# Performance work log

Hardware: AMD Instinct MI355X
Metric: run time of the kernel (lower is better)

Reference implementation:

```python
import jax, jax.numpy as jnp
import numpy as np

N = 2048

def setup_inputs() -> dict:
    key = jax.random.key(0)
    ks = jax.random.split(key, 7)
    x = jax.random.uniform(ks[0], (N,), dtype=jnp.float32) * 100.0  # time vector
    W1 = jax.random.normal(ks[1], (128, 2), dtype=jnp.float32) * 0.5
    b1 = jax.random.normal(ks[2], (128,), dtype=jnp.float32) * 0.1
    W2 = jax.random.normal(ks[3], (32, 128), dtype=jnp.float32) * 0.1
    b2 = jax.random.normal(ks[4], (32,), dtype=jnp.float32) * 0.1
    W3 = jax.random.normal(ks[5], (1, 32), dtype=jnp.float32) * 0.1
    b3 = jax.random.normal(ks[6], (1,), dtype=jnp.float32) * 0.1
    return {"x": x, "W1": W1, "b1": b1, "W2": W2, "b2": b2, "W3": W3, "b3": b3}

def reference(x, W1, b1, W2, b2, W3, b3):
    # Vectorized equivalent of the nested-loop pair build:
    # pairs (x[i], x[j]) for all j >= i (upper triangle incl. diagonal).
    n = x.shape[0]
    iu_r, iu_c = np.triu_indices(n)  # static index arrays, P = n(n+1)/2
    pairs = jnp.stack([x[iu_r], x[iu_c]], axis=-1)  # [P, 2]
    h = jax.nn.sigmoid(pairs @ W1.T + b1)           # [P, 128]
    h = jax.nn.relu(h @ W2.T + b2)                  # [P, 32]
    v = (h @ W3.T + b3)[:, 0]                       # [P]
    # K starts as eye; the loops overwrite the full upper triangle (incl. diag),
    # leaving the strictly-lower triangle at 0.
    K = jnp.zeros((n, n), dtype=x.dtype).at[iu_r, iu_c].set(v)
    return K.T @ K  # torch casts to double; kept float32 (jax x64 disabled)
```

## Files before the change

kernel.cpp:

```cpp
#include <hip/hip_runtime.h>
#include <hip/hip_bf16.h>

#define N 2048

using f32x4  = __attribute__((ext_vector_type(4))) float;
using short8 = __attribute__((ext_vector_type(8))) short;

#define GLOAD_LDS16(dst, src)                                                        \
  __builtin_amdgcn_global_load_lds((const __attribute__((address_space(1))) void*)(src), \
                                   (__attribute__((address_space(3))) void*)(dst), 16, 0, 0)

__device__ __forceinline__ short f2bf(float f) {
  unsigned u = __builtin_bit_cast(unsigned, f);
  u += 0x7fffu + ((u >> 16) & 1u);
  return (short)(u >> 16);
}

__global__ void w2_to_bf16(const float* __restrict__ W2, __hip_bfloat16* __restrict__ W2b) {
  int t = blockIdx.x * 256 + threadIdx.x;
  W2b[t] = __float2bfloat16(W2[t]);
}

__global__ __launch_bounds__(256) void build_A_mfma(
    const float* __restrict__ x,
    const float* __restrict__ W1,
    const float* __restrict__ b1,
    const __hip_bfloat16* __restrict__ W2b,
    const float* __restrict__ b2,
    const float* __restrict__ W3,
    const float* __restrict__ b3,
    __hip_bfloat16* __restrict__ A)
{
  const int bi = blockIdx.x, bj = blockIdx.y;
  const int i0 = bi * 16, j0 = bj * 16;
  const int tid = threadIdx.x;

  if (bi > bj) {
    A[(size_t)(j0 + (tid >> 4)) * N + i0 + (tid & 15)] = __float2bfloat16(0.0f);
    return;
  }

  __shared__ float w1s[256];
  __shared__ float b1s[128];
  w1s[tid] = W1[tid];
  if (tid < 128) b1s[tid] = b1[tid];
  __syncthreads();

  const int w  = tid >> 6;
  const int l  = tid & 63;
  const int lm = l & 15;
  const int lk = l >> 4;

  const float xi = x[i0 + lm];
  float xj[4];
#pragma unroll
  for (int m = 0; m < 4; ++m) xj[m] = x[j0 + w * 4 + m];

  short8 wf[2][4];
#pragma unroll
  for (int g = 0; g < 2; ++g)
#pragma unroll
    for (int kb = 0; kb < 4; ++kb)
      wf[g][kb] = *(const short8*)(W2b + (g * 16 + lm) * 128 + kb * 32 + lk * 8);

  float b2v[2] = {b2[lm], b2[16 + lm]};
  f32x4 acc[4][2];
#pragma unroll
  for (int m = 0; m < 4; ++m)
#pragma unroll
    for (int g = 0; g < 2; ++g)
      acc[m][g] = (f32x4){b2v[g], b2v[g], b2v[g], b2v[g]};

  for (int kb = 0; kb < 4; ++kb) {
    float w1a[8], w1b[8], bb[8];
#pragma unroll
    for (int e = 0; e < 8; ++e) {
      const int k = kb * 32 + lk * 8 + e;
      w1a[e] = w1s[2 * k];
      w1b[e] = w1s[2 * k + 1];
      bb[e]  = b1s[k];
    }
#pragma unroll
    for (int m = 0; m < 4; ++m) {
      short8 af;
#pragma unroll
      for (int e = 0; e < 8; ++e) {
        const float t  = fmaf(w1a[e], xi, fmaf(w1b[e], xj[m], bb[e]));
        const float ex = __expf(-t);
        const float h  = __builtin_amdgcn_rcpf(1.0f + ex);
        af[e] = f2bf(h);
      }
      acc[m][0] = __builtin_amdgcn_mfma_f32_16x16x32_bf16(af, wf[0][kb], acc[m][0], 0, 0, 0);
      acc[m][1] = __builtin_amdgcn_mfma_f32_16x16x32_bf16(af, wf[1][kb], acc[m][1], 0, 0, 0);
    }
  }

  const float w3a = W3[lm], w3b = W3[16 + lm];
  const float b3v = b3[0];
  const int   rsel = l & 3;

#pragma unroll
  for (int m = 0; m < 4; ++m) {
    const int j = j0 + w * 4 + m;
    float v[4];
#pragma unroll
    for (int r = 0; r < 4; ++r) {
      float s = fmaf(fmaxf(acc[m][0][r], 0.0f), w3a,
                     fmaxf(acc[m][1][r], 0.0f) * w3b);
      s += __shfl_xor(s, 1);
      s += __shfl_xor(s, 2);
      s += __shfl_xor(s, 4);
      s += __shfl_xor(s, 8);
      v[r] = s + b3v;
    }
    const float sv = rsel == 0 ? v[0] : rsel == 1 ? v[1] : rsel == 2 ? v[2] : v[3];
    if (lm < 4) {
      const int i = i0 + lk * 4 + rsel;
      A[(size_t)j * N + i] = (i <= j) ? __float2bfloat16(sv) : __float2bfloat16(0.0f);
    }
  }
}

__global__ __launch_bounds__(256) void gemm_ata(
    const __hip_bfloat16* __restrict__ A, float* __restrict__ C)
{
  __shared__ __align__(16) __hip_bfloat16 As[128 * 32];
  __shared__ __align__(16) __hip_bfloat16 Bs[128 * 32];

  const int m0 = blockIdx.y * 128;
  const int n0 = blockIdx.x * 128;
  const int tid = threadIdx.x;
  const int w  = tid >> 6;
  const int l  = tid & 63;
  const int wr = (w >> 1) * 64;
  const int wc = (w & 1) * 64;
  const int lm = l & 15;
  const int lk = l >> 4;

  f32x4 acc[4][4];
#pragma unroll
  for (int m = 0; m < 4; ++m)
#pragma unroll
    for (int n = 0; n < 4; ++n)
      acc[m][n] = (f32x4){0.f, 0.f, 0.f, 0.f};

  const int mn = m0 < n0 ? m0 : n0;
  const int ktiles = (mn + 128) >> 5;

  const int srow = l >> 2;
  const int scol = (l & 3) * 8;

  for (int kt = 0; kt < ktiles; ++kt) {
    const int k0 = kt * 32;
    __syncthreads();
#pragma unroll
    for (int c = 0; c < 2; ++c) {
      const int r0 = (w * 2 + c) * 16;
      const __hip_bfloat16* ga = A + (size_t)(m0 + r0 + srow) * N + k0 + scol;
      const __hip_bfloat16* gb = A + (size_t)(n0 + r0 + srow) * N + k0 + scol;
      GLOAD_LDS16(As + r0 * 32, ga);
      GLOAD_LDS16(Bs + r0 * 32, gb);
    }
    __syncthreads();

    short8 af[4], bfr[4];
#pragma unroll
    for (int m = 0; m < 4; ++m)
      af[m] = *(const short8*)(As + (wr + m * 16 + lm) * 32 + lk * 8);
#pragma unroll
    for (int n = 0; n < 4; ++n)
      bfr[n] = *(const short8*)(Bs + (wc + n * 16 + lm) * 32 + lk * 8);

#pragma unroll
    for (int m = 0; m < 4; ++m)
#pragma unroll
      for (int n = 0; n < 4; ++n)
        acc[m][n] = __builtin_amdgcn_mfma_f32_16x16x32_bf16(af[m], bfr[n], acc[m][n], 0, 0, 0);
  }

#pragma unroll
  for (int m = 0; m < 4; ++m) {
    const int row = m0 + wr + m * 16 + lk * 4;
#pragma unroll
    for (int n = 0; n < 4; ++n) {
      const int col = n0 + wc + n * 16 + lm;
#pragma unroll
      for (int r = 0; r < 4; ++r)
        C[(size_t)(row + r) * N + col] = acc[m][n][r];
    }
  }
}

extern "C" void kernel_launch(void* const* d_in, const int* in_sizes, int n_in,
                              void* d_out, int out_size, void* d_ws, size_t ws_size,
                              hipStream_t stream) {
  const float* x  = (const float*)d_in[0];
  const float* W1 = (const float*)d_in[1];
  const float* b1 = (const float*)d_in[2];
  const float* W2 = (const float*)d_in[3];
  const float* b2 = (const float*)d_in[4];
  const float* W3 = (const float*)d_in[5];
  const float* b3 = (const float*)d_in[6];
  float* C = (float*)d_out;

  __hip_bfloat16* W2b = (__hip_bfloat16*)d_ws;
  __hip_bfloat16* A   = (__hip_bfloat16*)((char*)d_ws + 16384);

  w2_to_bf16<<<dim3(16), dim3(256), 0, stream>>>(W2, W2b);
  build_A_mfma<<<dim3(N / 16, N / 16), dim3(256), 0, stream>>>(x, W1, b1, W2b, b2, W3, b3, A);
  gemm_ata<<<dim3(N / 128, N / 128), dim3(256), 0, stream>>>(A, C);
}
```

Baseline: 219.4 us.

## Triangular grid for A build, prescaled sigmoid, separate zero pass, smaller GEMM tiles

```diff
diff --git a/kernel.cpp b/kernel.cpp
--- a/kernel.cpp
+++ b/kernel.cpp
@@ -5,45 +5,50 @@
 
 using f32x4  = __attribute__((ext_vector_type(4))) float;
 using short8 = __attribute__((ext_vector_type(8))) short;
+using uint4v = __attribute__((ext_vector_type(4))) unsigned int;
 
 #define GLOAD_LDS16(dst, src)                                                        \
   __builtin_amdgcn_global_load_lds((const __attribute__((address_space(1))) void*)(src), \
                                    (__attribute__((address_space(3))) void*)(dst), 16, 0, 0)
 
-__device__ __forceinline__ short f2bf(float f) {
-  unsigned u = __builtin_bit_cast(unsigned, f);
-  u += 0x7fffu + ((u >> 16) & 1u);
-  return (short)(u >> 16);
-}
-
-__global__ void w2_to_bf16(const float* __restrict__ W2, __hip_bfloat16* __restrict__ W2b) {
+__global__ void prep(const float* __restrict__ W2, const float* __restrict__ W1,
+                     const float* __restrict__ b1,
+                     __hip_bfloat16* __restrict__ W2b,
+                     float* __restrict__ W1n, float* __restrict__ b1n) {
+  const float c = -1.4426950408889634f;
   int t = blockIdx.x * 256 + threadIdx.x;
   W2b[t] = __float2bfloat16(W2[t]);
+  if (t < 256) W1n[t] = W1[t] * c;
+  if (t < 128) b1n[t] = b1[t] * c;
+}
+
+__global__ void zero_A(uint4v* __restrict__ A4) {
+  A4[blockIdx.x * 256 + threadIdx.x] = (uint4v){0u, 0u, 0u, 0u};
 }
 
 __global__ __launch_bounds__(256) void build_A_mfma(
     const float* __restrict__ x,
-    const float* __restrict__ W1,
-    const float* __restrict__ b1,
+    const float* __restrict__ W1n,
+    const float* __restrict__ b1n,
     const __hip_bfloat16* __restrict__ W2b,
     const float* __restrict__ b2,
     const float* __restrict__ W3,
     const float* __restrict__ b3,
     __hip_bfloat16* __restrict__ A)
 {
-  const int bi = blockIdx.x, bj = blockIdx.y;
+  const int t = blockIdx.x;
+  int bj = (int)((sqrtf(8.0f * (float)t + 1.0f) - 1.0f) * 0.5f);
+  while ((bj + 1) * (bj + 2) / 2 <= t) ++bj;
+  while (bj * (bj + 1) / 2 > t) --bj;
+  const int bi = t - bj * (bj + 1) / 2;
+
   const int i0 = bi * 16, j0 = bj * 16;
   const int tid = threadIdx.x;
 
-  if (bi > bj) {
-    A[(size_t)(j0 + (tid >> 4)) * N + i0 + (tid & 15)] = __float2bfloat16(0.0f);
-    return;
-  }
-
   __shared__ float w1s[256];
   __shared__ float b1s[128];
-  w1s[tid] = W1[tid];
-  if (tid < 128) b1s[tid] = b1[tid];
+  w1s[tid] = W1n[tid & 255];
+  if (tid < 128) b1s[tid] = b1n[tid];
   __syncthreads();
 
   const int w  = tid >> 6;
@@ -63,7 +68,7 @@
     for (int kb = 0; kb < 4; ++kb)
       wf[g][kb] = *(const short8*)(W2b + (g * 16 + lm) * 128 + kb * 32 + lk * 8);
 
-  float b2v[2] = {b2[lm], b2[16 + lm]};
+  const float b2v[2] = {b2[lm], b2[16 + lm]};
   f32x4 acc[4][2];
 #pragma unroll
   for (int m = 0; m < 4; ++m)
@@ -71,25 +76,29 @@
     for (int g = 0; g < 2; ++g)
       acc[m][g] = (f32x4){b2v[g], b2v[g], b2v[g], b2v[g]};
 
+#pragma unroll
   for (int kb = 0; kb < 4; ++kb) {
-    float w1a[8], w1b[8], bb[8];
+    float base[8], w1b_[8];
 #pragma unroll
     for (int e = 0; e < 8; ++e) {
       const int k = kb * 32 + lk * 8 + e;
-      w1a[e] = w1s[2 * k];
-      w1b[e] = w1s[2 * k + 1];
-      bb[e]  = b1s[k];
+      base[e]  = fmaf(w1s[2 * k], xi, b1s[k]);
+      w1b_[e]  = w1s[2 * k + 1];
     }
 #pragma unroll
     for (int m = 0; m < 4; ++m) {
-      short8 af;
-#pragma unroll
-      for (int e = 0; e < 8; ++e) {
-        const float t  = fmaf(w1a[e], xi, fmaf(w1b[e], xj[m], bb[e]));
-        const float ex = __expf(-t);
-        const float h  = __builtin_amdgcn_rcpf(1.0f + ex);
-        af[e] = f2bf(h);
+      uint4v pk;
+#pragma unroll
+      for (int e2 = 0; e2 < 4; ++e2) {
+        const float t0 = fmaf(w1b_[2 * e2],     xj[m], base[2 * e2]);
+        const float t1 = fmaf(w1b_[2 * e2 + 1], xj[m], base[2 * e2 + 1]);
+        const float h0 = __builtin_amdgcn_rcpf(1.0f + __builtin_amdgcn_exp2f(t0));
+        const float h1 = __builtin_amdgcn_rcpf(1.0f + __builtin_amdgcn_exp2f(t1));
+        const unsigned u0 = __builtin_bit_cast(unsigned, h0) + 0x8000u;
+        const unsigned u1 = __builtin_bit_cast(unsigned, h1) + 0x8000u;
+        pk[e2] = __builtin_amdgcn_perm(u1, u0, 0x07060302u);
       }
+      const short8 af = __builtin_bit_cast(short8, pk);
       acc[m][0] = __builtin_amdgcn_mfma_f32_16x16x32_bf16(af, wf[0][kb], acc[m][0], 0, 0, 0);
       acc[m][1] = __builtin_amdgcn_mfma_f32_16x16x32_bf16(af, wf[1][kb], acc[m][1], 0, 0, 0);
     }
@@ -114,75 +123,68 @@
       v[r] = s + b3v;
     }
     const float sv = rsel == 0 ? v[0] : rsel == 1 ? v[1] : rsel == 2 ? v[2] : v[3];
-    if (lm < 4) {
-      const int i = i0 + lk * 4 + rsel;
-      A[(size_t)j * N + i] = (i <= j) ? __float2bfloat16(sv) : __float2bfloat16(0.0f);
-    }
+    const int i = i0 + lk * 4 + rsel;
+    if (lm < 4 && i <= j)
+      A[(size_t)j * N + i] = __float2bfloat16(sv);
   }
 }
 
 __global__ __launch_bounds__(256) void gemm_ata(
     const __hip_bfloat16* __restrict__ A, float* __restrict__ C)
 {
-  __shared__ __align__(16) __hip_bfloat16 As[128 * 32];
-  __shared__ __align__(16) __hip_bfloat16 Bs[128 * 32];
-
-  const int m0 = blockIdx.y * 128;
-  const int n0 = blockIdx.x * 128;
+  __shared__ __align__(16) __hip_bfloat16 As[64 * 32];
+  __shared__ __align__(16) __hip_bfloat16 Bs[64 * 32];
+
+  const int m0 = blockIdx.y * 64;
+  const int n0 = blockIdx.x * 64;
   const int tid = threadIdx.x;
   const int w  = tid >> 6;
   const int l  = tid & 63;
-  const int wr = (w >> 1) * 64;
-  const int wc = (w & 1) * 64;
+  const int wr = (w >> 1) * 32;
+  const int wc = (w & 1) * 32;
   const int lm = l & 15;
   const int lk = l >> 4;
 
-  f32x4 acc[4][4];
-#pragma unroll
-  for (int m = 0; m < 4; ++m)
-#pragma unroll
-    for (int n = 0; n < 4; ++n)
+  f32x4 acc[2][2];
+#pragma unroll
+  for (int m = 0; m < 2; ++m)
+#pragma unroll
+    for (int n = 0; n < 2; ++n)
       acc[m][n] = (f32x4){0.f, 0.f, 0.f, 0.f};
 
   const int mn = m0 < n0 ? m0 : n0;
-  const int ktiles = (mn + 128) >> 5;
-
-  const int srow = l >> 2;
+  const int ktiles = (mn + 64) >> 5;
+
+  const int srow = 16 * w + (l >> 2);
   const int scol = (l & 3) * 8;
 
   for (int kt = 0; kt < ktiles; ++kt) {
     const int k0 = kt * 32;
     __syncthreads();
-#pragma unroll
-    for (int c = 0; c < 2; ++c) {
-      const int r0 = (w * 2 + c) * 16;
-      const __hip_bfloat16* ga = A + (size_t)(m0 + r0 + srow) * N + k0 + scol;
-      const __hip_bfloat16* gb = A + (size_t)(n0 + r0 + srow) * N + k0 + scol;
-      GLOAD_LDS16(As + r0 * 32, ga);
-      GLOAD_LDS16(Bs + r0 * 32, gb);
-    }
+    GLOAD_LDS16(As + 16 * w * 32, A + (size_t)(m0 + srow) * N + k0 + scol);
+    GLOAD_LDS16(Bs + 16 * w * 32, A + (size_t)(n0 + srow) * N + k0 + scol);
     __syncthreads();
 
-    short8 af[4], bfr[4];
-#pragma unroll
-    for (int m = 0; m < 4; ++m)
+    short8 af[2], bfr[2];
+#pragma unroll
+    for (int m = 0; m < 2; ++m)
       af[m] = *(const short8*)(As + (wr + m * 16 + lm) * 32 + lk * 8);
 #pragma unroll
-    for (int n = 0; n < 4; ++n)
+    for (int n = 0; n < 2; ++n)
       bfr[n] = *(const short8*)(Bs + (wc + n * 16 + lm) * 32 + lk * 8);
 
 #pragma unroll
-    for (int m = 0; m < 4; ++m)
-#pragma unroll
-      for (int n = 0; n < 4; ++n)
+    for (int m = 0; m < 2; ++m)
+#pragma unroll
+      for (int n = 0; n < 2; ++n)
         acc[m][n] = __builtin_amdgcn_mfma_f32_16x16x32_bf16(af[m], bfr[n], acc[m][n], 0, 0, 0);
   }
 
 #pragma unroll
-  for (int m = 0; m < 4; ++m) {
+  for (int m = 0; m < 2; ++m) {
     const int row = m0 + wr + m * 16 + lk * 4;
 #pragma unroll
-    for (int n = 0; n < 4; ++n) {
+    for (int n = 0; n < 2; ++n) {
       const int col = n0 + wc + n * 16 + lm;
 #pragma unroll
       for (int r = 0; r < 4; ++r)
@@ -204,9 +206,12 @@
   float* C = (float*)d_out;
 
   __hip_bfloat16* W2b = (__hip_bfloat16*)d_ws;
-  __hip_bfloat16* A   = (__hip_bfloat16*)((char*)d_ws + 16384);
-
-  w2_to_bf16<<<dim3(16), dim3(256), 0, stream>>>(W2, W2b);
-  build_A_mfma<<<dim3(N / 16, N / 16), dim3(256), 0, stream>>>(x, W1, b1, W2b, b2, W3, b3, A);
-  gemm_ata<<<dim3(N / 128, N / 128), dim3(256), 0, stream>>>(A, C);
-}
+  float* W1n = (float*)((char*)d_ws + 8192);
+  float* b1n = (float*)((char*)d_ws + 12288);
+  __hip_bfloat16* A = (__hip_bfloat16*)((char*)d_ws + 16384);
+
+  prep<<<dim3(16), dim3(256), 0, stream>>>(W2, W1, b1, W2b, W1n, b1n);
+  zero_A<<<dim3(2048), dim3(256), 0, stream>>>((uint4v*)A);
+  build_A_mfma<<<dim3(8256), dim3(256), 0, stream>>>(x, W1n, b1n, W2b, b2, W3, b3, A);
+  gemm_ata<<<dim3(32, 32), dim3(256), 0, stream>>>(A, C);
+}
```

Measured after the change: 179.0 us. -18.4%, faster.
